# Kernel tuning notes

Measured on AMD Instinct MI355X. Metric: run time of the kernel, lower is better.

## Reference

```python
import jax, jax.numpy as jnp
import numpy as np

B, C, D = 16384, 512, 512
EXT = 2
H = C * EXT
TAU = 1.0          # temperature_train
STEP = 0.05        # langevin_step_size
NOISE = 0.1        # langevin_noise
STEPS = 32         # langevin_steps


def setup_inputs() -> dict:
    key = jax.random.key(0)
    ks = jax.random.split(key, 8)
    s_in = 1.0 / np.sqrt(D)
    s_h = 1.0 / np.sqrt(H)
    return {
        'x': jax.random.normal(ks[0], (B, D), jnp.float32),
        'vanilla_components': jnp.abs(jax.random.normal(ks[1], (C, D), jnp.float32) * 0.1),
        'e_sp': jax.random.normal(ks[2], (C * D,), jnp.float32) * 0.1,
        'W1e': jax.random.normal(ks[3], (D, H), jnp.float32) * s_in,
        'b1e': jnp.zeros((H,), jnp.float32),
        'W2e': jax.random.normal(ks[4], (H, C), jnp.float32) * s_h,
        'b2e': jnp.zeros((C,), jnp.float32),
        'W1r': jax.random.normal(ks[5], (D, H), jnp.float32) * s_in,
        'b1r': jnp.zeros((H,), jnp.float32),
        'W2r': jax.random.normal(ks[6], (H, C), jnp.float32) * s_h,
        'b2r': jnp.zeros((C,), jnp.float32),
    }


def _langevin_gate(e, key):
    """Langevin MCMC on latent u with quadratic energy E(u)=0.5||u||^2 + <e,u>.
    Returns selection probability sigmoid(-u/tau)."""
    def step(u, k):
        grad = u + e  # dE/du
        u = u - STEP * grad + NOISE * jax.random.normal(k, u.shape, u.dtype)
        return u, None
    u, _ = jax.lax.scan(step, jnp.zeros_like(e), jax.random.split(key, STEPS))
    return jax.nn.sigmoid(-u / TAU)


def reference(x, vanilla_components, e_sp, W1e, b1e, W2e, b2e, W1r, b1r, W2r, b2r):
    k1, k2 = jax.random.split(jax.random.key(42))
    # non-negative components
    comps = jnp.abs(vanilla_components)  # [C, D]
    # fixed energy-based sparsity mask over component entries
    p_sp = _langevin_gate(e_sp, k1).reshape(C, D)
    comps = comps * p_sp
    # dynamic per-sample component selection energies via MLP
    h = jax.nn.relu(x @ W1e + b1e)          # [B, H]
    e_dyn = h @ W2e + b2e                   # [B, C]
    gate = _langevin_gate(e_dyn, k2)        # [B, C] soft gates (train mode)
    hr = jax.nn.relu(x @ W1r + b1r)         # [B, H]
    conc = (hr @ W2r + b2r) * gate          # [B, C]
    # aggregate: (concentration * components).sum over components -> [B, D]
    return conc @ comps
```

## Files before the change

kernel.cpp:

```cpp
#include <hip/hip_runtime.h>
#include <hip/hip_bf16.h>
#include <stdint.h>

#define Bn 16384
#define Cn 512
#define Dn 512
#define Hn 1024

#define A32 0.80628851f

typedef __attribute__((ext_vector_type(8))) short bf16x8;
typedef __attribute__((ext_vector_type(4))) float f32x4;
typedef __attribute__((ext_vector_type(2))) float f32x2;

__device__ __forceinline__ ushort f2bf(float f) {
  uint32_t u = __float_as_uint(f);
  return (ushort)((u + 0x7fffu + ((u >> 16) & 1u)) >> 16);
}
__device__ __forceinline__ float b2f(ushort u) {
  return __uint_as_float((uint32_t)u << 16);
}

typedef __attribute__((address_space(3))) uint32_t lds_u32_t;
typedef const __attribute__((address_space(1))) uint32_t glb_u32_t;
__device__ __forceinline__ void gload16(const ushort* g, ushort* l) {
  __builtin_amdgcn_global_load_lds((glb_u32_t*)g, (lds_u32_t*)l, 16, 0, 0);
}

constexpr uint32_t crotl(uint32_t v, int s) {
  return (v << s) | (v >> (32 - s));
}
struct TFOut { uint32_t w0, w1; };
constexpr TFOut ctf(uint32_t k0, uint32_t k1, uint32_t x0, uint32_t x1) {
  const uint32_t ks[3] = {k0, k1, k0 ^ k1 ^ 0x1BD11BDAu};
  const int rot[8] = {13, 15, 26, 6, 17, 29, 16, 24};
  uint32_t a = x0 + k0, b = x1 + k1;
  for (int g = 0; g < 5; ++g) {
    for (int i = 0; i < 4; ++i) {
      int r = rot[(g & 1) * 4 + i];
      a += b; b = crotl(b, r); b ^= a;
    }
    a += ks[(g + 1) % 3];
    b += ks[(g + 2) % 3] + (uint32_t)(g + 1);
  }
  return {a, b};
}
struct KeySched { uint32_t s[64]; uint32_t d[64]; };
constexpr KeySched make_keys() {
  KeySched K{};
  TFOut k1 = ctf(0u, 42u, 0u, 0u);
  TFOut k2 = ctf(0u, 42u, 0u, 1u);
  for (uint32_t t = 0; t < 32; ++t) {
    TFOut ws = ctf(k1.w0, k1.w1, 0u, t);
    K.s[2 * t] = ws.w0; K.s[2 * t + 1] = ws.w1;
    TFOut wd = ctf(k2.w0, k2.w1, 0u, t);
    K.d[2 * t] = wd.w0; K.d[2 * t + 1] = wd.w1;
  }
  return K;
}
__constant__ KeySched KS = make_keys();

__device__ __forceinline__ uint32_t rotl32(uint32_t v, int s) {
  return __builtin_rotateleft32(v, (uint32_t)s);
}
__device__ __forceinline__ uint32_t tf_xor(uint32_t K0, uint32_t K1,
                                           uint32_t KX, uint32_t j) {
  uint32_t a = K0, b = K1 + j;
#define TR(r) { a += b; b = rotl32(b, (r)); b ^= a; }
  TR(13) TR(15) TR(26) TR(6)   a += K1; b += KX + 1u;
  TR(17) TR(29) TR(16) TR(24)  a += KX; b += K0 + 2u;
  TR(13) TR(15) TR(26) TR(6)   a += K0; b += K1 + 3u;
  TR(17) TR(29) TR(16) TR(24)  a += K1; b += KX + 4u;
  TR(13) TR(15) TR(26) TR(6)   a += KX; b += K0 + 5u;
#undef TR
  return a ^ b;
}

__device__ __forceinline__ float bits_to_normal(uint32_t bits) {
  float f = __uint_as_float((bits >> 9) | 0x3f800000u) - 1.0f;
  float x = f * 2.0f - 0x1.fffffep-1f;
  float w = -__logf(1.0f - x * x);
  float p;
  if (w < 5.0f) {
    w -= 2.5f;
    p =            2.81022636e-08f;
    p = fmaf(p, w, 3.43273939e-07f);
    p = fmaf(p, w, -3.5233877e-06f);
    p = fmaf(p, w, -4.39150654e-06f);
    p = fmaf(p, w, 0.00021858087f);
    p = fmaf(p, w, -0.00125372503f);
    p = fmaf(p, w, -0.00417768164f);
    p = fmaf(p, w, 0.246640727f);
    p = fmaf(p, w, 1.50140941f);
  } else {
    w = sqrtf(w) - 3.0f;
    p =            -0.000200214257f;
    p = fmaf(p, w, 0.000100950558f);
    p = fmaf(p, w, 0.00134934322f);
    p = fmaf(p, w, -0.00367342844f);
    p = fmaf(p, w, 0.00573950773f);
    p = fmaf(p, w, -0.0076224613f);
    p = fmaf(p, w, 0.00943887047f);
    p = fmaf(p, w, 1.00167406f);
    p = fmaf(p, w, 2.83297682f);
  }
  return 0x1.6a09e6p+0f * (p * x);
}

__device__ __forceinline__ void z_block(ushort* __restrict__ Z, uint32_t zidx) {
  const uint32_t j0 = (zidx * 256u + threadIdx.x) * 2u;
  const uint32_t j1 = j0 + 1u;
  float z0 = 0.0f, z1 = 0.0f;
#pragma unroll 4
  for (int t = 0; t < 32; ++t) {
    const uint32_t K0 = KS.d[2 * t], K1 = KS.d[2 * t + 1];
    const uint32_t KX = K0 ^ K1 ^ 0x1BD11BDAu;
    uint32_t a0 = K0, b0 = K1 + j0;
    uint32_t a1 = K0, b1 = K1 + j1;
#define R2(r)                                                  \
    a0 += b0; a1 += b1;                                        \
    b0 = rotl32(b0, (r)); b1 = rotl32(b1, (r));                \
    b0 ^= a0; b1 ^= a1;
#define I2(p, q) a0 += (p); a1 += (p); b0 += (q); b1 += (q);
    R2(13) R2(15) R2(26) R2(6)  I2(K1, KX + 1u)
    R2(17) R2(29) R2(16) R2(24) I2(KX, K0 + 2u)
    R2(13) R2(15) R2(26) R2(6)  I2(K0, K1 + 3u)
    R2(17) R2(29) R2(16) R2(24) I2(K1, KX + 4u)
    R2(13) R2(15) R2(26) R2(6)  I2(KX, K0 + 5u)
#undef R2
#undef I2
    uint32_t s0 = a0 ^ b0, s1 = a1 ^ b1;
    float f0 = __uint_as_float((s0 >> 9) | 0x3f800000u) - 1.0f;
    float f1 = __uint_as_float((s1 >> 9) | 0x3f800000u) - 1.0f;
    float x0 = f0 * 2.0f - 0x1.fffffep-1f;
    float x1 = f1 * 2.0f - 0x1.fffffep-1f;
    float w0 = fminf(-__logf(fmaf(-x0, x0, 1.0f)), 5.0f) - 2.5f;
    float w1 = fminf(-__logf(fmaf(-x1, x1, 1.0f)), 5.0f) - 2.5f;
    f32x2 X = {x0, x1}, W = {w0, w1};
    f32x2 P = {2.81022636e-08f, 2.81022636e-08f};
    P = __builtin_elementwise_fma(P, W, (f32x2){3.43273939e-07f, 3.43273939e-07f});
    P = __builtin_elementwise_fma(P, W, (f32x2){-3.5233877e-06f, -3.5233877e-06f});
    P = __builtin_elementwise_fma(P, W, (f32x2){-4.39150654e-06f, -4.39150654e-06f});
    P = __builtin_elementwise_fma(P, W, (f32x2){0.00021858087f, 0.00021858087f});
    P = __builtin_elementwise_fma(P, W, (f32x2){-0.00125372503f, -0.00125372503f});
    P = __builtin_elementwise_fma(P, W, (f32x2){-0.00417768164f, -0.00417768164f});
    P = __builtin_elementwise_fma(P, W, (f32x2){0.246640727f, 0.246640727f});
    P = __builtin_elementwise_fma(P, W, (f32x2){1.50140941f, 1.50140941f});
    f32x2 Q = (P * X) * (f32x2){0.14142135f, 0.14142135f};
    z0 = fmaf(0.95f, z0, Q.x);
    z1 = fmaf(0.95f, z1, Q.y);
  }
  *(ushort2*)(Z + j0) = make_ushort2(f2bf(z0), f2bf(z1));
}

__device__ __forceinline__ void transpose_tile(
    const float* __restrict__ in, ushort* __restrict__ out,
    int N, int K, int tIdx, float T[32][33]) {
  const int ntn = N / 32;
  const int tk = tIdx / ntn, tn = tIdx % ntn;
  const int tx = threadIdx.x & 31, ty = threadIdx.x >> 5;
  const int k0 = tk * 32, n0 = tn * 32;
#pragma unroll
  for (int r = 0; r < 32; r += 8)
    T[ty + r][tx] = in[(size_t)(k0 + ty + r) * N + n0 + tx];
  __syncthreads();
#pragma unroll
  for (int r = 0; r < 32; r += 8)
    out[(size_t)(n0 + ty + r) * K + k0 + tx] = f2bf(T[tx][ty + r]);
}

__device__ __forceinline__ void smask_block(
    const float* __restrict__ vc, const float* __restrict__ e_sp,
    ushort* __restrict__ compsT, int g) {
  uint32_t jj = (uint32_t)g * 256 + threadIdx.x;
  uint32_t c = jj & (Cn - 1), d = jj >> 9;
  uint32_t ridx = c * Dn + d;
  float e = e_sp[ridx];
  float u = 0.0f;
#pragma unroll 4
  for (int t = 0; t < 32; ++t) {
    const uint32_t K0 = KS.s[2 * t], K1 = KS.s[2 * t + 1];
    uint32_t s = tf_xor(K0, K1, K0 ^ K1 ^ 0x1BD11BDAu, ridx);
    float n = bits_to_normal(s);
    u = (u - 0.05f * (u + e)) + 0.1f * n;
  }
  float gt = 1.0f / (1.0f + __expf(u));
  compsT[jj] = f2bf(fabsf(vc[ridx]) * gt);
}

__global__ __launch_bounds__(256, 8) void k_prep_z(
    const float* __restrict__ x, ushort* __restrict__ x_bf,
    const float* __restrict__ W1e, ushort* __restrict__ W1eT,
    const float* __restrict__ W2e, ushort* __restrict__ W2eT,
    const float* __restrict__ W1r, ushort* __restrict__ W1rT,
    const float* __restrict__ W2r, ushort* __restrict__ W2rT,
    const float* __restrict__ vc, const float* __restrict__ e_sp,
    ushort* __restrict__ compsT, ushort* __restrict__ Zd) {
  __shared__ float T[32][33];
  const int pos = blockIdx.x;
  if ((pos % 5) == 4) {
    z_block(Zd, (uint32_t)(pos / 5));
    return;
  }
  const int p = (pos / 5) * 4 + (pos % 5);
  if (p < 8192) {
    int i = (p * 256 + threadIdx.x) * 4;
    float4 v = *(const float4*)(x + i);
    *(ushort4*)(x_bf + i) =
        make_ushort4(f2bf(v.x), f2bf(v.y), f2bf(v.z), f2bf(v.w));
  } else if (p < 8704) {
    transpose_tile(W1e, W1eT, Hn, Dn, p - 8192, T);
  } else if (p < 9216) {
    transpose_tile(W2e, W2eT, Cn, Hn, p - 8704, T);
  } else if (p < 9728) {
    transpose_tile(W1r, W1rT, Hn, Dn, p - 9216, T);
  } else if (p < 10240) {
    transpose_tile(W2r, W2rT, Cn, Hn, p - 9728, T);
  } else {
    smask_block(vc, e_sp, compsT, p - 10240);
  }
}

__device__ __forceinline__ void gemm_core64(
    const ushort* __restrict__ A, const ushort* __restrict__ WT,
    int m0, int n0, int LD, int K,
    ushort* __restrict__ AsL, ushort* __restrict__ BsL,
    f32x4 acc[2][2]) {
  const int t = threadIdx.x;
  const int wave = t >> 6, lane = t & 63;
  const int row = t >> 2;
  const int col8 = ((t & 3) << 3) ^ (((t >> 3) & 3) << 3);
  const int wr = (wave >> 1) << 5, wc = (wave & 1) << 5;
  const int quad = lane >> 4, l15 = lane & 15;
  const int rc = (quad << 3) ^ (((l15 >> 1) & 3) << 3);

  const ushort* ga = A  + (size_t)(m0 + row) * LD + col8;
  const ushort* gb = WT + (size_t)(n0 + row) * LD + col8;
  ushort* la = AsL + wave * 512;
  ushort* lb = BsL + wave * 512;

  for (int k0 = 0; k0 < K; k0 += 32) {
    gload16(ga + k0, la);
    gload16(gb + k0, lb);
    __syncthreads();
    bf16x8 af[2], bfr[2];
#pragma unroll
    for (int i = 0; i < 2; ++i) {
      af[i]  = *(const bf16x8*)&AsL[(wr + i * 16 + l15) * 32 + rc];
      bfr[i] = *(const bf16x8*)&BsL[(wc + i * 16 + l15) * 32 + rc];
    }
#pragma unroll
    for (int i = 0; i < 2; ++i)
#pragma unroll
      for (int j = 0; j < 2; ++j)
        acc[i][j] = __builtin_amdgcn_mfma_f32_16x16x32_bf16(af[i], bfr[j],
                                                            acc[i][j], 0, 0, 0);
    __syncthreads();
  }
}

__device__ __forceinline__ void gemm_tile_bf64(
    const ushort* __restrict__ A, const ushort* __restrict__ WT,
    const float* __restrict__ bias, ushort* __restrict__ Out,
    int m0, int n0, ushort* AsL, ushort* BsL) {
  const int t = threadIdx.x;
  const int wave = t >> 6, lane = t & 63;
  const int wr = (wave >> 1) << 5, wc = (wave & 1) << 5;
  const int quad = lane >> 4, l15 = lane & 15;
  f32x4 acc[2][2] = {};
  gemm_core64(A, WT, m0, n0, Dn, Dn, AsL, BsL, acc);
#pragma unroll
  for (int i = 0; i < 2; ++i)
#pragma unroll
    for (int j = 0; j < 2; ++j) {
      const int col = n0 + wc + j * 16 + l15;
      const float bv = bias[col];
#pragma unroll
      for (int r = 0; r < 4; ++r) {
        const int row = m0 + wr + i * 16 + quad * 4 + r;
        Out[(size_t)row * Hn + col] = f2bf(fmaxf(acc[i][j][r] + bv, 0.0f));
      }
    }
}

__global__ __launch_bounds__(256, 8) void k_g13_z(
    const ushort* __restrict__ x_bf,
    const ushort* __restrict__ W1eT, const float* __restrict__ b1e,
    ushort* __restrict__ h,
    const ushort* __restrict__ W1rT, const float* __restrict__ b1r,
    ushort* __restrict__ hr, ushort* __restrict__ Zd) {
  __shared__ ushort AsL[2048];
  __shared__ ushort BsL[2048];
  const int pos = blockIdx.x;
  if ((pos % 3) == 2) {
    z_block(Zd, 2816u + (uint32_t)(pos / 3));
    return;
  }
  const int gg = (pos / 3) * 2 + (pos % 3);
  const int g = gg >> 1;
  const int m0 = (g >> 4) * 64, n0 = (g & 15) * 64;
  if (gg & 1)
    gemm_tile_bf64(x_bf, W1rT, b1r, hr, m0, n0, AsL, BsL);
  else
    gemm_tile_bf64(x_bf, W1eT, b1e, h, m0, n0, AsL, BsL);
}

__device__ __forceinline__ void gemm_tile_f32out64(
    const ushort* __restrict__ A, const ushort* __restrict__ WT,
    const float* __restrict__ bias, float* __restrict__ Out,
    int m0, int n0, ushort* AsL, ushort* BsL) {
  const int t = threadIdx.x;
  const int wave = t >> 6, lane = t & 63;
  const int wr = (wave >> 1) << 5, wc = (wave & 1) << 5;
  const int quad = lane >> 4, l15 = lane & 15;
  f32x4 acc[2][2] = {};
  gemm_core64(A, WT, m0, n0, Hn, Hn, AsL, BsL, acc);
#pragma unroll
  for (int i = 0; i < 2; ++i)
#pragma unroll
    for (int j = 0; j < 2; ++j) {
      const int col = n0 + wc + j * 16 + l15;
      const float bv = bias[col];
#pragma unroll
      for (int r = 0; r < 4; ++r) {
        const int row = m0 + wr + i * 16 + quad * 4 + r;
        Out[(size_t)row * Cn + col] = acc[i][j][r] + bv;
      }
    }
}

__global__ __launch_bounds__(256, 8) void k_e_z(
    const ushort* __restrict__ h, const ushort* __restrict__ W2eT,
    const float* __restrict__ b2e, float* __restrict__ e_out,
    ushort* __restrict__ Zd) {
  __shared__ ushort AsL[2048];
  __shared__ ushort BsL[2048];
  const int pos = blockIdx.x;
  if ((pos % 13) < 4) {
    const int tg = (pos / 13) * 4 + (pos % 13);
    gemm_tile_f32out64(h, W2eT, b2e, e_out, (tg >> 3) * 64, (tg & 7) * 64,
                       AsL, BsL);
  } else {
    z_block(Zd, 6912u + (uint32_t)((pos / 13) * 9 + (pos % 13) - 4));
  }
}

__global__ __launch_bounds__(256, 8) void k_r_z(
    const ushort* __restrict__ hr, const ushort* __restrict__ W2rT,
    const float* __restrict__ b2r, float* __restrict__ cr_out,
    ushort* __restrict__ Zd) {
  __shared__ ushort AsL[2048];
  __shared__ ushort BsL[2048];
  const int pos = blockIdx.x;
  if ((pos % 27) < 8) {
    const int tg = (pos / 27) * 8 + (pos % 27);
    gemm_tile_f32out64(hr, W2rT, b2r, cr_out, (tg >> 3) * 64, (tg & 7) * 64,
                       AsL, BsL);
  } else {
    z_block(Zd, 11520u + (uint32_t)((pos / 27) * 19 + (pos % 27) - 8));
  }
}

__global__ __launch_bounds__(256) void k_gate(
    const float* __restrict__ e, const float* __restrict__ cr,
    ushort* __restrict__ Z) {
  const size_t i = ((size_t)blockIdx.x * 256u + threadIdx.x) * 8u;
  uint4 zv = *(const uint4*)(Z + i);
  ushort zs[8];
  *(uint4*)zs = zv;
  float ee[8], cc[8];
  *(float4*)(ee)     = *(const float4*)(e + i);
  *(float4*)(ee + 4) = *(const float4*)(e + i + 4);
  *(float4*)(cc)     = *(const float4*)(cr + i);
  *(float4*)(cc + 4) = *(const float4*)(cr + i + 4);
  ushort os[8];
#pragma unroll
  for (int k = 0; k < 8; ++k) {
    float z = b2f(zs[k]);
    float g = 1.0f / (1.0f + __expf(z - A32 * ee[k]));
    os[k] = f2bf(cc[k] * g);
  }
  *(uint4*)(Z + i) = *(uint4*)os;
}

__device__ __forceinline__ void stage4(
    const ushort* ga0, const ushort* ga1,
    const ushort* gb0, const ushort* gb1,
    int k, ushort* As, ushort* Bs, int wo) {
  gload16(ga0 + k, As + wo);
  gload16(ga1 + k, As + 2048 + wo);
  gload16(gb0 + k, Bs + wo);
  gload16(gb1 + k, Bs + 2048 + wo);
}

__device__ __forceinline__ void mfma16(
    const ushort* Ac, const ushort* Bc,
    int wm, int wn, int l15, int rc, f32x4 acc[4][4]) {
  bf16x8 af[4], bfr[4];
#pragma unroll
  for (int i = 0; i < 4; ++i) {
    af[i]  = *(const bf16x8*)&Ac[(wm + i * 16 + l15) * 32 + rc];
    bfr[i] = *(const bf16x8*)&Bc[(wn + i * 16 + l15) * 32 + rc];
  }
#pragma unroll
  for (int i = 0; i < 4; ++i)
#pragma unroll
    for (int j = 0; j < 4; ++j)
      acc[i][j] = __builtin_amdgcn_mfma_f32_16x16x32_bf16(af[i], bfr[j],
                                                          acc[i][j], 0, 0, 0);
}

__global__ __launch_bounds__(256) void k_gemm_out(
    const ushort* __restrict__ A, const ushort* __restrict__ WT,
    float* __restrict__ Out) {
  __shared__ ushort As0[4096];
  __shared__ ushort Bs0[4096];
  __shared__ ushort As1[4096];
  __shared__ ushort Bs1[4096];
  const int t = threadIdx.x;
  const int m0 = blockIdx.y * 128, n0 = blockIdx.x * 128;
  const int wave = t >> 6, lane = t & 63;
  const int row = t >> 2;
  const int col8 = ((t & 3) << 3) ^ (((t >> 3) & 3) << 3);
  const int wm = (wave >> 1) << 6, wn = (wave & 1) << 6;
  const int quad = lane >> 4, l15 = lane & 15;
  const int rc = (quad << 3) ^ (((l15 >> 1) & 3) << 3);
  const int wo = wave * 512;

  const ushort* ga0 = A  + (size_t)(m0 + row) * Cn + col8;
  const ushort* ga1 = A  + (size_t)(m0 + 64 + row) * Cn + col8;
  const ushort* gb0 = WT + (size_t)(n0 + row) * Cn + col8;
  const ushort* gb1 = WT + (size_t)(n0 + 64 + row) * Cn + col8;

  f32x4 acc[4][4] = {};
  stage4(ga0, ga1, gb0, gb1, 0, As0, Bs0, wo);
  for (int k0 = 0; k0 < Cn; k0 += 64) {
    stage4(ga0, ga1, gb0, gb1, k0 + 32, As1, Bs1, wo);
    asm volatile("s_waitcnt vmcnt(4)" ::: "memory");
    __builtin_amdgcn_sched_barrier(0);
    __builtin_amdgcn_s_barrier();
    mfma16(As0, Bs0, wm, wn, l15, rc, acc);
    __builtin_amdgcn_s_barrier();
    if (k0 + 64 < Cn) {
      stage4(ga0, ga1, gb0, gb1, k0 + 64, As0, Bs0, wo);
      asm volatile("s_waitcnt vmcnt(4)" ::: "memory");
    } else {
      asm volatile("s_waitcnt vmcnt(0)" ::: "memory");
    }
    __builtin_amdgcn_sched_barrier(0);
    __builtin_amdgcn_s_barrier();
    mfma16(As1, Bs1, wm, wn, l15, rc, acc);
    __builtin_amdgcn_s_barrier();
  }
#pragma unroll
  for (int i = 0; i < 4; ++i)
#pragma unroll
    for (int j = 0; j < 4; ++j) {
      const int col = n0 + wn + j * 16 + l15;
#pragma unroll
      for (int r = 0; r < 4; ++r) {
        const int row2 = m0 + wm + i * 16 + quad * 4 + r;
        Out[(size_t)row2 * Dn + col] = acc[i][j][r];
      }
    }
}

extern "C" void kernel_launch(void* const* d_in, const int* in_sizes, int n_in,
                              void* d_out, int out_size, void* d_ws, size_t ws_size,
                              hipStream_t stream) {
  const float* x    = (const float*)d_in[0];
  const float* vc   = (const float*)d_in[1];
  const float* e_sp = (const float*)d_in[2];
  const float* W1e  = (const float*)d_in[3];
  const float* b1e  = (const float*)d_in[4];
  const float* W2e  = (const float*)d_in[5];
  const float* b2e  = (const float*)d_in[6];
  const float* W1r  = (const float*)d_in[7];
  const float* b1r  = (const float*)d_in[8];
  const float* W2r  = (const float*)d_in[9];
  const float* b2r  = (const float*)d_in[10];
  float* out = (float*)d_out;

  char* ws = (char*)d_ws;
  ushort* W1eT   = (ushort*)(ws + (1u << 12));
  ushort* W2eT   = (ushort*)(ws + (1u << 12) + (1u << 20));
  ushort* W1rT   = (ushort*)(ws + (1u << 12) + (2u << 20));
  ushort* W2rT   = (ushort*)(ws + (1u << 12) + (3u << 20));
  ushort* compsT = (ushort*)(ws + (1u << 12) + (4u << 20));
  ushort* Zdyn   = (ushort*)(ws + (8u << 20));
  ushort* h_bf   = (ushort*)(ws + (24u << 20));
  ushort* hr_bf  = (ushort*)(ws + (56u << 20));
  float*  cr_f32 = (float*)(ws + (24u << 20));
  ushort* x_bf   = (ushort*)d_out;
  float*  e_f32  = (float*)d_out;

  k_prep_z<<<14080, 256, 0, stream>>>(x, x_bf, W1e, W1eT, W2e, W2eT,
                                      W1r, W1rT, W2r, W2rT, vc, e_sp, compsT,
                                      Zdyn);
  k_g13_z<<<12288, 256, 0, stream>>>(x_bf, W1eT, b1e, h_bf, W1rT, b1r, hr_bf,
                                     Zdyn);
  k_e_z<<<6656, 256, 0, stream>>>(h_bf, W2eT, b2e, e_f32, Zdyn);
  k_r_z<<<6912, 256, 0, stream>>>(hr_bf, W2rT, b2r, cr_f32, Zdyn);
  k_gate<<<4096, 256, 0, stream>>>(e_f32, cr_f32, Zdyn);
  k_gemm_out<<<dim3(Dn / 128, Bn / 128), 256, 0, stream>>>(Zdyn, compsT, out);
}
```

Before: 844.6 us.

## Interleave Langevin noise generation inside GEMM k-loop with larger 128x128 tiles

The GEMM kernels move from 256-thread 64x64 tiles to 512-thread 128x128 tiles. Each GEMM block now also computes part of the dynamic-gate noise (Threefry plus inverse-erf) inside its k-loop, so the ALU work overlaps with MFMA and memory latency. Before, separate z-only blocks were mixed into the grid. The goal is better MFMA utilisation and more data reuse per tile. In exchange, the fused loop uses more registers, and the launch bounds and z-index ranges are rebalanced.

New measurement: 817.8 us. -3.2%, faster.

```diff
diff --git a/kernel.cpp b/kernel.cpp
--- a/kernel.cpp
+++ b/kernel.cpp
@@ -107,49 +107,61 @@
   return 0x1.6a09e6p+0f * (p * x);
 }
 
+__device__ __forceinline__ void z_step(int t, uint32_t j0, uint32_t j1,
+                                       float& z0, float& z1) {
+  const uint32_t K0 = KS.d[2 * t], K1 = KS.d[2 * t + 1];
+  const uint32_t KX = K0 ^ K1 ^ 0x1BD11BDAu;
+  uint32_t a0 = K0, b0 = K1 + j0;
+  uint32_t a1 = K0, b1 = K1 + j1;
+#define R2(r)                                                  \
+  a0 += b0; a1 += b1;                                          \
+  b0 = rotl32(b0, (r)); b1 = rotl32(b1, (r));                  \
+  b0 ^= a0; b1 ^= a1;
+#define I2(p, q) a0 += (p); a1 += (p); b0 += (q); b1 += (q);
+  R2(13) R2(15) R2(26) R2(6)  I2(K1, KX + 1u)
+  R2(17) R2(29) R2(16) R2(24) I2(KX, K0 + 2u)
+  R2(13) R2(15) R2(26) R2(6)  I2(K0, K1 + 3u)
+  R2(17) R2(29) R2(16) R2(24) I2(K1, KX + 4u)
+  R2(13) R2(15) R2(26) R2(6)  I2(KX, K0 + 5u)
+#undef R2
+#undef I2
+  uint32_t s0 = a0 ^ b0, s1 = a1 ^ b1;
+  float f0 = __uint_as_float((s0 >> 9) | 0x3f800000u) - 1.0f;
+  float f1 = __uint_as_float((s1 >> 9) | 0x3f800000u) - 1.0f;
+  float x0 = f0 * 2.0f - 0x1.fffffep-1f;
+  float x1 = f1 * 2.0f - 0x1.fffffep-1f;
+  float w0 = fminf(-__logf(fmaf(-x0, x0, 1.0f)), 5.0f) - 2.5f;
+  float w1 = fminf(-__logf(fmaf(-x1, x1, 1.0f)), 5.0f) - 2.5f;
+  f32x2 X = {x0, x1}, W = {w0, w1};
+  f32x2 P = {2.81022636e-08f, 2.81022636e-08f};
+  P = __builtin_elementwise_fma(P, W, (f32x2){3.43273939e-07f, 3.43273939e-07f});
+  P = __builtin_elementwise_fma(P, W, (f32x2){-3.5233877e-06f, -3.5233877e-06f});
+  P = __builtin_elementwise_fma(P, W, (f32x2){-4.39150654e-06f, -4.39150654e-06f});
+  P = __builtin_elementwise_fma(P, W, (f32x2){0.00021858087f, 0.00021858087f});
+  P = __builtin_elementwise_fma(P, W, (f32x2){-0.00125372503f, -0.00125372503f});
+  P = __builtin_elementwise_fma(P, W, (f32x2){-0.00417768164f, -0.00417768164f});
+  P = __builtin_elementwise_fma(P, W, (f32x2){0.246640727f, 0.246640727f});
+  P = __builtin_elementwise_fma(P, W, (f32x2){1.50140941f, 1.50140941f});
+  f32x2 Q = (P * X) * (f32x2){0.14142135f, 0.14142135f};
+  z0 = fmaf(0.95f, z0, Q.x);
+  z1 = fmaf(0.95f, z1, Q.y);
+}
+
 __device__ __forceinline__ void z_block(ushort* __restrict__ Z, uint32_t zidx) {
   const uint32_t j0 = (zidx * 256u + threadIdx.x) * 2u;
   const uint32_t j1 = j0 + 1u;
   float z0 = 0.0f, z1 = 0.0f;
 #pragma unroll 4
-  for (int t = 0; t < 32; ++t) {
-    const uint32_t K0 = KS.d[2 * t], K1 = KS.d[2 * t + 1];
-    const uint32_t KX = K0 ^ K1 ^ 0x1BD11BDAu;
-    uint32_t a0 = K0, b0 = K1 + j0;
-    uint32_t a1 = K0, b1 = K1 + j1;
-#define R2(r)                                                  \
-    a0 += b0; a1 += b1;                                        \
-    b0 = rotl32(b0, (r)); b1 = rotl32(b1, (r));                \
-    b0 ^= a0; b1 ^= a1;
-#define I2(p, q) a0 += (p); a1 += (p); b0 += (q); b1 += (q);
-    R2(13) R2(15) R2(26) R2(6)  I2(K1, KX + 1u)
-    R2(17) R2(29) R2(16) R2(24) I2(KX, K0 + 2u)
-    R2(13) R2(15) R2(26) R2(6)  I2(K0, K1 + 3u)
-    R2(17) R2(29) R2(16) R2(24) I2(K1, KX + 4u)
-    R2(13) R2(15) R2(26) R2(6)  I2(KX, K0 + 5u)
-#undef R2
-#undef I2
-    uint32_t s0 = a0 ^ b0, s1 = a1 ^ b1;
-    float f0 = __uint_as_float((s0 >> 9) | 0x3f800000u) - 1.0f;
-    float f1 = __uint_as_float((s1 >> 9) | 0x3f800000u) - 1.0f;
-    float x0 = f0 * 2.0f - 0x1.fffffep-1f;
-    float x1 = f1 * 2.0f - 0x1.fffffep-1f;
-    float w0 = fminf(-__logf(fmaf(-x0, x0, 1.0f)), 5.0f) - 2.5f;
-    float w1 = fminf(-__logf(fmaf(-x1, x1, 1.0f)), 5.0f) - 2.5f;
-    f32x2 X = {x0, x1}, W = {w0, w1};
-    f32x2 P = {2.81022636e-08f, 2.81022636e-08f};
-    P = __builtin_elementwise_fma(P, W, (f32x2){3.43273939e-07f, 3.43273939e-07f});
-    P = __builtin_elementwise_fma(P, W, (f32x2){-3.5233877e-06f, -3.5233877e-06f});
-    P = __builtin_elementwise_fma(P, W, (f32x2){-4.39150654e-06f, -4.39150654e-06f});
-    P = __builtin_elementwise_fma(P, W, (f32x2){0.00021858087f, 0.00021858087f});
-    P = __builtin_elementwise_fma(P, W, (f32x2){-0.00125372503f, -0.00125372503f});
-    P = __builtin_elementwise_fma(P, W, (f32x2){-0.00417768164f, -0.00417768164f});
-    P = __builtin_elementwise_fma(P, W, (f32x2){0.246640727f, 0.246640727f});
-    P = __builtin_elementwise_fma(P, W, (f32x2){1.50140941f, 1.50140941f});
-    f32x2 Q = (P * X) * (f32x2){0.14142135f, 0.14142135f};
-    z0 = fmaf(0.95f, z0, Q.x);
-    z1 = fmaf(0.95f, z1, Q.y);
-  }
+  for (int t = 0; t < 32; ++t) z_step(t, j0, j1, z0, z1);
+  *(ushort2*)(Z + j0) = make_ushort2(f2bf(z0), f2bf(z1));
+}
+
+__device__ __forceinline__ void z_unit512(ushort* __restrict__ Z, uint32_t u) {
+  const uint32_t j0 = 1441792u + u * 1024u + (uint32_t)threadIdx.x * 2u;
+  const uint32_t j1 = j0 + 1u;
+  float z0 = 0.0f, z1 = 0.0f;
+#pragma unroll 4
+  for (int t = 0; t < 32; ++t) z_step(t, j0, j1, z0, z1);
   *(ushort2*)(Z + j0) = make_ushort2(f2bf(z0), f2bf(z1));
 }
 
@@ -188,7 +200,7 @@
   compsT[jj] = f2bf(fabsf(vc[ridx]) * gt);
 }
 
-__global__ __launch_bounds__(256, 8) void k_prep_z(
+__global__ __launch_bounds__(256) void k_prep_z(
     const float* __restrict__ x, ushort* __restrict__ x_bf,
     const float* __restrict__ W1e, ushort* __restrict__ W1eT,
     const float* __restrict__ W2e, ushort* __restrict__ W2eT,
@@ -221,17 +233,18 @@
   }
 }
 
-__device__ __forceinline__ void gemm_core64(
+template <int KIT, int ZS>
+__device__ __forceinline__ void gemm_z_fused(
     const ushort* __restrict__ A, const ushort* __restrict__ WT,
-    int m0, int n0, int LD, int K,
+    int m0, int n0, int LD,
     ushort* __restrict__ AsL, ushort* __restrict__ BsL,
-    f32x4 acc[2][2]) {
+    f32x4 acc[4][2], uint32_t j0, uint32_t j1, float& z0, float& z1) {
   const int t = threadIdx.x;
   const int wave = t >> 6, lane = t & 63;
   const int row = t >> 2;
   const int col8 = ((t & 3) << 3) ^ (((t >> 3) & 3) << 3);
-  const int wr = (wave >> 1) << 5, wc = (wave & 1) << 5;
-  const int quad = lane >> 4, l15 = lane & 15;
+  const int wm = (wave >> 2) << 6, wn = (wave & 3) << 5;
+  const int l15 = lane & 15, quad = lane >> 4;
   const int rc = (quad << 3) ^ (((l15 >> 1) & 3) << 3);
 
   const ushort* ga = A  + (size_t)(m0 + row) * LD + col8;
@@ -239,126 +252,142 @@
   ushort* la = AsL + wave * 512;
   ushort* lb = BsL + wave * 512;
 
-  for (int k0 = 0; k0 < K; k0 += 32) {
-    gload16(ga + k0, la);
-    gload16(gb + k0, lb);
+  for (int it = 0; it < KIT; ++it) {
+    gload16(ga + it * 32, la);
+    gload16(gb + it * 32, lb);
     __syncthreads();
-    bf16x8 af[2], bfr[2];
-#pragma unroll
-    for (int i = 0; i < 2; ++i) {
-      af[i]  = *(const bf16x8*)&AsL[(wr + i * 16 + l15) * 32 + rc];
-      bfr[i] = *(const bf16x8*)&BsL[(wc + i * 16 + l15) * 32 + rc];
-    }
-#pragma unroll
-    for (int i = 0; i < 2; ++i)
+    bf16x8 af[4], bfr[2];
+#pragma unroll
+    for (int i = 0; i < 4; ++i)
+      af[i] = *(const bf16x8*)&AsL[(wm + i * 16 + l15) * 32 + rc];
+#pragma unroll
+    for (int j = 0; j < 2; ++j)
+      bfr[j] = *(const bf16x8*)&BsL[(wn + j * 16 + l15) * 32 + rc];
+#pragma unroll
+    for (int i = 0; i < 4; ++i)
 #pragma unroll
       for (int j = 0; j < 2; ++j)
         acc[i][j] = __builtin_amdgcn_mfma_f32_16x16x32_bf16(af[i], bfr[j],
                                                             acc[i][j], 0, 0, 0);
+#pragma unroll
+    for (int s = 0; s < ZS; ++s)
+      z_step(it * ZS + s, j0, j1, z0, z1);
     __syncthreads();
   }
 }
 
-__device__ __forceinline__ void gemm_tile_bf64(
-    const ushort* __restrict__ A, const ushort* __restrict__ WT,
-    const float* __restrict__ bias, ushort* __restrict__ Out,
-    int m0, int n0, ushort* AsL, ushort* BsL) {
-  const int t = threadIdx.x;
-  const int wave = t >> 6, lane = t & 63;
-  const int wr = (wave >> 1) << 5, wc = (wave & 1) << 5;
-  const int quad = lane >> 4, l15 = lane & 15;
-  f32x4 acc[2][2] = {};
-  gemm_core64(A, WT, m0, n0, Dn, Dn, AsL, BsL, acc);
-#pragma unroll
-  for (int i = 0; i < 2; ++i)
-#pragma unroll
-    for (int j = 0; j < 2; ++j) {
-      const int col = n0 + wc + j * 16 + l15;
-      const float bv = bias[col];
-#pragma unroll
-      for (int r = 0; r < 4; ++r) {
-        const int row = m0 + wr + i * 16 + quad * 4 + r;
-        Out[(size_t)row * Hn + col] = f2bf(fmaxf(acc[i][j][r] + bv, 0.0f));
-      }
-    }
-}
-
-__global__ __launch_bounds__(256, 8) void k_g13_z(
+__global__ __launch_bounds__(512, 6) void k_g13_z(
     const ushort* __restrict__ x_bf,
     const ushort* __restrict__ W1eT, const float* __restrict__ b1e,
     ushort* __restrict__ h,
     const ushort* __restrict__ W1rT, const float* __restrict__ b1r,
     ushort* __restrict__ hr, ushort* __restrict__ Zd) {
-  __shared__ ushort AsL[2048];
-  __shared__ ushort BsL[2048];
+  __shared__ ushort AsL[4096];
+  __shared__ ushort BsL[4096];
   const int pos = blockIdx.x;
-  if ((pos % 3) == 2) {
-    z_block(Zd, 2816u + (uint32_t)(pos / 3));
+  if (pos >= 2048) {
+    z_unit512(Zd, (uint32_t)pos);
     return;
   }
-  const int gg = (pos / 3) * 2 + (pos % 3);
-  const int g = gg >> 1;
-  const int m0 = (g >> 4) * 64, n0 = (g & 15) * 64;
-  if (gg & 1)
-    gemm_tile_bf64(x_bf, W1rT, b1r, hr, m0, n0, AsL, BsL);
-  else
-    gemm_tile_bf64(x_bf, W1eT, b1e, h, m0, n0, AsL, BsL);
-}
-
-__device__ __forceinline__ void gemm_tile_f32out64(
-    const ushort* __restrict__ A, const ushort* __restrict__ WT,
-    const float* __restrict__ bias, float* __restrict__ Out,
-    int m0, int n0, ushort* AsL, ushort* BsL) {
-  const int t = threadIdx.x;
-  const int wave = t >> 6, lane = t & 63;
-  const int wr = (wave >> 1) << 5, wc = (wave & 1) << 5;
+  const uint32_t j0 = 1441792u + (uint32_t)pos * 1024u +
+                      (uint32_t)threadIdx.x * 2u;
+  const uint32_t j1 = j0 + 1u;
+  float z0 = 0.0f, z1 = 0.0f;
+  const int tg = pos >> 1;
+  const int m0 = (tg >> 3) * 128, n0 = (tg & 7) * 128;
+  const ushort* WTp = (pos & 1) ? W1rT : W1eT;
+  const float*  bp  = (pos & 1) ? b1r  : b1e;
+  ushort*       Op  = (pos & 1) ? hr   : h;
+  f32x4 acc[4][2] = {};
+  gemm_z_fused<16, 2>(x_bf, WTp, m0, n0, Dn, AsL, BsL, acc, j0, j1, z0, z1);
+  *(ushort2*)(Zd + j0) = make_ushort2(f2bf(z0), f2bf(z1));
+  const int wave = threadIdx.x >> 6, lane = threadIdx.x & 63;
+  const int wm = (wave >> 2) << 6, wn = (wave & 3) << 5;
   const int quad = lane >> 4, l15 = lane & 15;
-  f32x4 acc[2][2] = {};
-  gemm_core64(A, WT, m0, n0, Hn, Hn, AsL, BsL, acc);
-#pragma unroll
-  for (int i = 0; i < 2; ++i)
+#pragma unroll
+  for (int i = 0; i < 4; ++i)
 #pragma unroll
     for (int j = 0; j < 2; ++j) {
-      const int col = n0 + wc + j * 16 + l15;
-      const float bv = bias[col];
+      const int col = n0 + wn + j * 16 + l15;
+      const float bv = bp[col];
 #pragma unroll
       for (int r = 0; r < 4; ++r) {
-        const int row = m0 + wr + i * 16 + quad * 4 + r;
-        Out[(size_t)row * Cn + col] = acc[i][j][r] + bv;
+        const int row = m0 + wm + i * 16 + quad * 4 + r;
+        Op[(size_t)row * Hn + col] = f2bf(fmaxf(acc[i][j][r] + bv, 0.0f));
       }
     }
 }
 
-__global__ __launch_bounds__(256, 8) void k_e_z(
+__global__ __launch_bounds__(512, 6) void k_e_z(
     const ushort* __restrict__ h, const ushort* __restrict__ W2eT,
     const float* __restrict__ b2e, float* __restrict__ e_out,
     ushort* __restrict__ Zd) {
-  __shared__ ushort AsL[2048];
-  __shared__ ushort BsL[2048];
+  __shared__ ushort AsL[4096];
+  __shared__ ushort BsL[4096];
   const int pos = blockIdx.x;
-  if ((pos % 13) < 4) {
-    const int tg = (pos / 13) * 4 + (pos % 13);
-    gemm_tile_f32out64(h, W2eT, b2e, e_out, (tg >> 3) * 64, (tg & 7) * 64,
-                       AsL, BsL);
-  } else {
-    z_block(Zd, 6912u + (uint32_t)((pos / 13) * 9 + (pos % 13) - 4));
-  }
-}
-
-__global__ __launch_bounds__(256, 8) void k_r_z(
+  const uint32_t u = 3072u + (uint32_t)pos;
+  if (pos >= 512) {
+    z_unit512(Zd, u);
+    return;
+  }
+  const uint32_t j0 = 1441792u + u * 1024u + (uint32_t)threadIdx.x * 2u;
+  const uint32_t j1 = j0 + 1u;
+  float z0 = 0.0f, z1 = 0.0f;
+  const int m0 = (pos >> 2) * 128, n0 = (pos & 3) * 128;
+  f32x4 acc[4][2] = {};
+  gemm_z_fused<32, 1>(h, W2eT, m0, n0, Hn, AsL, BsL, acc, j0, j1, z0, z1);
+  *(ushort2*)(Zd + j0) = make_ushort2(f2bf(z0), f2bf(z1));
+  const int wave = threadIdx.x >> 6, lane = threadIdx.x & 63;
+  const int wm = (wave >> 2) << 6, wn = (wave & 3) << 5;
+  const int quad = lane >> 4, l15 = lane & 15;
+#pragma unroll
+  for (int i = 0; i < 4; ++i)
+#pragma unroll
+    for (int j = 0; j < 2; ++j) {
+      const int col = n0 + wn + j * 16 + l15;
+      const float bv = b2e[col];
+#pragma unroll
+      for (int r = 0; r < 4; ++r) {
+        const int row = m0 + wm + i * 16 + quad * 4 + r;
+        e_out[(size_t)row * Cn + col] = acc[i][j][r] + bv;
+      }
+    }
+}
+
+__global__ __launch_bounds__(512, 6) void k_r_z(
     const ushort* __restrict__ hr, const ushort* __restrict__ W2rT,
     const float* __restrict__ b2r, float* __restrict__ cr_out,
     ushort* __restrict__ Zd) {
-  __shared__ ushort AsL[2048];
-  __shared__ ushort BsL[2048];
+  __shared__ ushort AsL[4096];
+  __shared__ ushort BsL[4096];
   const int pos = blockIdx.x;
-  if ((pos % 27) < 8) {
-    const int tg = (pos / 27) * 8 + (pos % 27);
-    gemm_tile_f32out64(hr, W2rT, b2r, cr_out, (tg >> 3) * 64, (tg & 7) * 64,
-                       AsL, BsL);
-  } else {
-    z_block(Zd, 11520u + (uint32_t)((pos / 27) * 19 + (pos % 27) - 8));
-  }
+  const uint32_t u = 4928u + (uint32_t)pos;
+  if (pos >= 512) {
+    z_unit512(Zd, u);
+    return;
+  }
+  const uint32_t j0 = 1441792u + u * 1024u + (uint32_t)threadIdx.x * 2u;
+  const uint32_t j1 = j0 + 1u;
+  float z0 = 0.0f, z1 = 0.0f;
+  const int m0 = (pos >> 2) * 128, n0 = (pos & 3) * 128;
+  f32x4 acc[4][2] = {};
+  gemm_z_fused<32, 1>(hr, W2rT, m0, n0, Hn, AsL, BsL, acc, j0, j1, z0, z1);
+  *(ushort2*)(Zd + j0) = make_ushort2(f2bf(z0), f2bf(z1));
+  const int wave = threadIdx.x >> 6, lane = threadIdx.x & 63;
+  const int wm = (wave >> 2) << 6, wn = (wave & 3) << 5;
+  const int quad = lane >> 4, l15 = lane & 15;
+#pragma unroll
+  for (int i = 0; i < 4; ++i)
+#pragma unroll
+    for (int j = 0; j < 2; ++j) {
+      const int col = n0 + wn + j * 16 + l15;
+      const float bv = b2r[col];
+#pragma unroll
+      for (int r = 0; r < 4; ++r) {
+        const int row = m0 + wm + i * 16 + quad * 4 + r;
+        cr_out[(size_t)row * Cn + col] = acc[i][j][r] + bv;
+      }
+    }
 }
 
 __global__ __launch_bounds__(256) void k_gate(
@@ -497,10 +526,10 @@
   k_prep_z<<<14080, 256, 0, stream>>>(x, x_bf, W1e, W1eT, W2e, W2eT,
                                       W1r, W1rT, W2r, W2rT, vc, e_sp, compsT,
                                       Zdyn);
-  k_g13_z<<<12288, 256, 0, stream>>>(x_bf, W1eT, b1e, h_bf, W1rT, b1r, hr_bf,
-                                     Zdyn);
-  k_e_z<<<6656, 256, 0, stream>>>(h_bf, W2eT, b2e, e_f32, Zdyn);
-  k_r_z<<<6912, 256, 0, stream>>>(hr_bf, W2rT, b2r, cr_f32, Zdyn);
+  k_g13_z<<<3072, 512, 0, stream>>>(x_bf, W1eT, b1e, h_bf, W1rT, b1r, hr_bf,
+                                    Zdyn);
+  k_e_z<<<1856, 512, 0, stream>>>(h_bf, W2eT, b2e, e_f32, Zdyn);
+  k_r_z<<<1856, 512, 0, stream>>>(hr_bf, W2rT, b2r, cr_f32, Zdyn);
   k_gate<<<4096, 256, 0, stream>>>(e_f32, cr_f32, Zdyn);
   k_gemm_out<<<dim3(Dn / 128, Bn / 128), 256, 0, stream>>>(Zdyn, compsT, out);
 }
```
